# Kernel tuning notes

Hardware: AMD Instinct MI355X
Metric: run time of the kernel (lower is better)

Reference implementation:

```python
import jax, jax.numpy as jnp
import numpy as np

N = 100000   # nodes
E = 1600000  # edges
G = 64       # graphs in batch
D = 128      # node_dim
H = 128      # hid_dim
OUT = 10     # out_dim (classes)
L = 3        # max_layer GIN layers per branch
BN_EPS = 1e-5


def setup_inputs() -> dict:
    key = jax.random.key(0)
    ks = jax.random.split(key, 24)
    p = lambda k, shape: (jax.random.normal(k, shape, jnp.float32) * 0.05)
    inp = {
        "x": jax.random.normal(ks[0], (N, D), jnp.float32),
        "edge_index": jax.random.randint(ks[1], (2, E), 0, N, jnp.int32),
        "batch": jnp.sort(jax.random.randint(ks[2], (N,), 0, G, jnp.int32)),
        # branch A: conv1 + convs  (stacked per-layer params; node_dim == hid_dim)
        "W1a": p(ks[3], (L, D, H)), "b1a": p(ks[4], (L, H)),
        "W2a": p(ks[5], (L, H, H)), "b2a": p(ks[6], (L, H)),
        "ga": jnp.ones((L, H), jnp.float32), "bta": jnp.zeros((L, H), jnp.float32),
        # branch B: conv2 + convs2
        "W1b": p(ks[7], (L, D, H)), "b1b": p(ks[8], (L, H)),
        "W2b": p(ks[9], (L, H, H)), "b2b": p(ks[10], (L, H)),
        "gb": jnp.ones((L, H), jnp.float32), "btb": jnp.zeros((L, H), jnp.float32),
        # heads
        "lin1_w": p(ks[11], (2 * H, H)), "lin1_b": p(ks[12], (H,)),
        "lin2_w": p(ks[13], (H, OUT)), "lin2_b": p(ks[14], (OUT,)),
        # bilinear discriminator (nn.Bilinear(H, H, 1))
        "disc_w": p(ks[15], (H, H)), "disc_b": jnp.zeros((), jnp.float32),
    }
    return inp


def _gin(h, src, dst, W1, b1, W2, b2, g, bt):
    # GINConv (eps=0): MLP(x + sum_{j->i} x_j); MLP = Lin-ReLU-Lin-ReLU-BN
    agg = jax.ops.segment_sum(h[src], dst, num_segments=N)  # scatter-add over edges
    h = h + agg
    h = jax.nn.relu(h @ W1 + b1)
    h = jax.nn.relu(h @ W2 + b2)
    mu = h.mean(0)
    var = jnp.mean((h - mu) ** 2, axis=0)
    return (h - mu) * jax.lax.rsqrt(var + BN_EPS) * g + bt


def reference(x, edge_index, batch, W1a, b1a, W2a, b2a, ga, bta,
              W1b, b1b, W2b, b2b, gb, btb, lin1_w, lin1_b, lin2_w, lin2_b,
              disc_w, disc_b):
    src, dst = edge_index[0], edge_index[1]
    counts = jnp.clip(jax.ops.segment_sum(jnp.ones((N,), x.dtype), batch, num_segments=G), 1.0)

    # branch A: conv1 + convs -> per-graph mean pool
    h = x
    for i in range(L):
        h = _gin(h, src, dst, W1a[i], b1a[i], W2a[i], b2a[i], ga[i], bta[i])
    mean_a = jax.ops.segment_sum(h, batch, num_segments=G) / counts[:, None]  # [G,H]

    # branch B (subgraph branch, run on the same graph): conv2 + convs2 -> pool
    hb = x
    for i in range(L):
        hb = _gin(hb, src, dst, W1b[i], b1b[i], W2b[i], b2b[i], gb[i], btb[i])
    pool_x = jax.ops.segment_sum(hb, batch, num_segments=G) / counts[:, None]  # [G,H]

    # MI discriminator: shuffle index as in Net.MI
    idx = jnp.arange(G - 1, -1, -1)
    idx = idx.at[G // 2].set(idx[G // 2 + 1])
    shuffled = pool_x[idx]
    bil = lambda a, c: jnp.einsum('gd,de,ge->g', a, disc_w, c) + disc_b
    logits = jnp.concatenate([bil(pool_x, pool_x), bil(pool_x, shuffled)])  # [2G]

    # classification head: cat(mean_pool, pool_x) -> lin1 -> relu -> lin2 -> log_softmax
    z = jnp.concatenate([mean_a, pool_x], axis=-1)
    z = jax.nn.relu(z @ lin1_w + lin1_b)
    z = z @ lin2_w + lin2_b
    predicts = jax.nn.log_softmax(z, axis=-1)  # [G,OUT]

    return jnp.concatenate([predicts.ravel(), logits.ravel()])  # [G*OUT + 2G]
```

## Files before the change

### kernel.cpp

```cpp
#include <hip/hip_runtime.h>
#include <hip/hip_bf16.h>

#define NN 100000
#define EE 1600000
#define GG 64
#define HH 128
#define LL 3
#define BN_EPS 1e-5f
#define NBUCK 196
#define BCAP 12288
#define PART_CHUNK 8192

typedef __attribute__((ext_vector_type(8))) short bf16x8;
typedef __attribute__((ext_vector_type(4))) float f32x4;
typedef unsigned int uint32;

__device__ __forceinline__ float bflo(uint32 u) { return __uint_as_float(u << 16); }
__device__ __forceinline__ float bfhi(uint32 u) { return __uint_as_float(u & 0xffff0000u); }
__device__ __forceinline__ unsigned short f2bf(float f) {
    uint32 x = __float_as_uint(f);
    uint32 r = (x + 0x7fffu + ((x >> 16) & 1u)) >> 16;
    return (unsigned short)r;
}
__device__ __forceinline__ float bf2f(unsigned short u) { return __uint_as_float(((uint32)u) << 16); }
__device__ __forceinline__ void acc2(float2& a, uint32 u) { a.x += bflo(u); a.y += bfhi(u); }
__device__ __forceinline__ void accq(float4& a, uint32 u, float sc) {
    a.x += sc * (float)(u & 0xffu);
    a.y += sc * (float)((u >> 8) & 0xffu);
    a.z += sc * (float)((u >> 16) & 0xffu);
    a.w += sc * (float)(u >> 24);
}

__global__ __launch_bounds__(256) void partition_kernel(
    const int* __restrict__ src, const int* __restrict__ dst,
    int* __restrict__ bcnt, uint32* __restrict__ part) {
    __shared__ int cnt[NBUCK];
    __shared__ int loff[NBUCK + 1];
    __shared__ int gpos[NBUCK];
    __shared__ int lcur[NBUCK];
    __shared__ uint32 buf[PART_CHUNK];
    int tid = threadIdx.x;
    int base = blockIdx.x * PART_CHUNK;
    int n = min(PART_CHUNK, EE - base);
    for (int i = tid; i < NBUCK; i += 256) { cnt[i] = 0; lcur[i] = 0; }
    __syncthreads();
    for (int i = tid; i < n; i += 256) atomicAdd(&cnt[dst[base + i] >> 9], 1);
    __syncthreads();
    if (tid == 0) {
        int acc = 0;
        for (int b = 0; b < NBUCK; ++b) { loff[b] = acc; acc += cnt[b]; }
        loff[NBUCK] = acc;
    }
    __syncthreads();
    if (tid < NBUCK && cnt[tid] > 0) gpos[tid] = atomicAdd(&bcnt[tid], cnt[tid]);
    __syncthreads();
    for (int i = tid; i < n; i += 256) {
        int d = dst[base + i];
        int s = src[base + i];
        int b = d >> 9;
        int slot = atomicAdd(&lcur[b], 1);
        buf[loff[b] + slot] = (uint32)s | ((uint32)(d & 511) << 17);
    }
    __syncthreads();
    for (int i = tid; i < n; i += 256) {
        int lo = 0, hi = NBUCK;
        while (hi - lo > 1) { int mid = (lo + hi) >> 1; if (loff[mid] <= i) lo = mid; else hi = mid; }
        part[(size_t)lo * BCAP + gpos[lo] + (i - loff[lo])] = buf[i];
    }
}

__global__ __launch_bounds__(256) void build_col_kernel(
    const uint32* __restrict__ part, const int* __restrict__ bcnt,
    int* __restrict__ col, int2* __restrict__ rowpair) {
    __shared__ int ldeg[512];
    __shared__ int loffn[512];
    __shared__ int lcur[512];
    __shared__ int pscan[256];
    __shared__ int cl[BCAP];
    int b = blockIdx.x;
    int tid = threadIdx.x;
    int node0 = b << 9;
    int nn = min(node0 + 512, NN) - node0;
    int cnt = bcnt[b];
    int base = b * BCAP;
    const uint32* pp = part + (size_t)base;
    for (int i = tid; i < 512; i += 256) { ldeg[i] = 0; lcur[i] = 0; }
    __syncthreads();
    for (int i = tid; i < cnt; i += 256) atomicAdd(&ldeg[pp[i] >> 17], 1);
    __syncthreads();
    int t2 = tid * 2;
    int a0 = ldeg[t2], a1 = ldeg[t2 + 1];
    int ps = a0 + a1;
    pscan[tid] = ps;
    __syncthreads();
    for (int off = 1; off < 256; off <<= 1) {
        int v = (tid >= off) ? pscan[tid - off] : 0;
        __syncthreads();
        pscan[tid] += v;
        __syncthreads();
    }
    int eo = pscan[tid] - ps;
    loffn[t2] = eo;
    loffn[t2 + 1] = eo + a0;
    if (t2 < nn)     rowpair[node0 + t2]     = make_int2(base + eo, base + eo + a0);
    if (t2 + 1 < nn) rowpair[node0 + t2 + 1] = make_int2(base + eo + a0, base + eo + a0 + a1);
    __syncthreads();
    for (int i = tid; i < cnt; i += 256) {
        uint32 v = pp[i];
        int dl = (int)(v >> 17);
        int pos = atomicAdd(&lcur[dl], 1);
        cl[loffn[dl] + pos] = (int)(v & 0x1FFFFu);
    }
    __syncthreads();
    for (int i = tid; i < cnt; i += 256) col[base + i] = cl[i];
}

__global__ void counts_kernel(const int* __restrict__ batch, float* __restrict__ cnt, int n) {
    __shared__ int h[GG];
    int tid = threadIdx.x;
    if (tid < GG) h[tid] = 0;
    __syncthreads();
    int i = blockIdx.x * 256 + tid;
    if (i < n) atomicAdd(&h[batch[i]], 1);
    __syncthreads();
    if (tid < GG && h[tid]) atomicAdd(&cnt[tid], (float)h[tid]);
}

__global__ void x_to_bf16_kernel(const float* __restrict__ x, uint32* __restrict__ xb) {
    int i = blockIdx.x * 256 + threadIdx.x;
    if (i < NN * 32) {
        float4 v = ((const float4*)x)[i];
        uint2 o;
        o.x = (uint32)f2bf(v.x) | ((uint32)f2bf(v.y) << 16);
        o.y = (uint32)f2bf(v.z) | ((uint32)f2bf(v.w) << 16);
        ((uint2*)xb)[i] = o;
    }
}

#define MAT_STRIDE 16384

__global__ void convert_w_kernel(const float* __restrict__ W1a, const float* __restrict__ W2a,
                                 const float* __restrict__ W1b, const float* __restrict__ W2b,
                                 unsigned short* __restrict__ out) {
    int t = blockIdx.x * 256 + threadIdx.x;
    if (t >= 24576) return;
    int lane = t & 63;
    int r = t >> 6;
    int ks = r & 3; r >>= 2;
    int nt = r & 7; r >>= 3;
    int mat = r & 1; r >>= 1;
    int l = r % 3, br = r / 3;
    const float* W = br ? (mat ? W2b : W1b) : (mat ? W2a : W1a);
    const float* Wl = W + (size_t)l * 128 * 128;
    int n0 = nt * 16 + (lane & 15);
    int k0 = ks * 32 + (lane >> 4) * 8;
    unsigned short tmp[8];
#pragma unroll
    for (int j = 0; j < 8; ++j) tmp[j] = f2bf(Wl[(size_t)(k0 + j) * 128 + n0]);
    size_t seq = (size_t)(br * 3 + l) * 2 + mat;
    size_t off = (((seq * 8 + nt) * 4 + ks) * 64 + (size_t)lane) * 8;
    *(uint4*)(out + off) = *(const uint4*)tmp;
}

__global__ void gather0_kernel(const uint4* __restrict__ h4, const int2* __restrict__ rowpair,
                               const int* __restrict__ col, uint4* __restrict__ out) {
    int gw = (blockIdx.x * blockDim.x + threadIdx.x) >> 6;
    int lane = threadIdx.x & 63;
    if (gw >= NN) return;
    int slot = lane >> 4;
    int c8 = lane & 15;
    float2 acc[4] = {{0.f,0.f},{0.f,0.f},{0.f,0.f},{0.f,0.f}};
    if (slot == 0) {
        uint4 s = h4[(size_t)gw * 16 + c8];
        acc2(acc[0], s.x); acc2(acc[1], s.y); acc2(acc[2], s.z); acc2(acc[3], s.w);
    }
    int2 be = rowpair[gw];
    int beg = be.x, end = be.y;
    int e = beg;
    for (; e + 8 <= end; e += 8) {
        int j0 = col[e + slot], j1 = col[e + 4 + slot];
        uint4 u0 = h4[(size_t)j0 * 16 + c8];
        uint4 u1 = h4[(size_t)j1 * 16 + c8];
        acc2(acc[0], u0.x); acc2(acc[1], u0.y); acc2(acc[2], u0.z); acc2(acc[3], u0.w);
        acc2(acc[0], u1.x); acc2(acc[1], u1.y); acc2(acc[2], u1.z); acc2(acc[3], u1.w);
    }
    for (; e + 4 <= end; e += 4) {
        int j = col[e + slot];
        uint4 u = h4[(size_t)j * 16 + c8];
        acc2(acc[0], u.x); acc2(acc[1], u.y); acc2(acc[2], u.z); acc2(acc[3], u.w);
    }
    int rem = end - e;
    if (slot < rem) {
        int j = col[e + slot];
        uint4 u = h4[(size_t)j * 16 + c8];
        acc2(acc[0], u.x); acc2(acc[1], u.y); acc2(acc[2], u.z); acc2(acc[3], u.w);
    }
#pragma unroll
    for (int k = 0; k < 4; ++k) {
        acc[k].x += __shfl_xor(acc[k].x, 16); acc[k].y += __shfl_xor(acc[k].y, 16);
        acc[k].x += __shfl_xor(acc[k].x, 32); acc[k].y += __shfl_xor(acc[k].y, 32);
    }
    if (slot == 0) {
        uint4 r;
        r.x = (uint32)f2bf(acc[0].x) | ((uint32)f2bf(acc[0].y) << 16);
        r.y = (uint32)f2bf(acc[1].x) | ((uint32)f2bf(acc[1].y) << 16);
        r.z = (uint32)f2bf(acc[2].x) | ((uint32)f2bf(acc[2].y) << 16);
        r.w = (uint32)f2bf(acc[3].x) | ((uint32)f2bf(acc[3].y) << 16);
        out[(size_t)gw * 16 + c8] = r;
    }
}

__global__ void gather_dual_kernel(const uint32* __restrict__ y8, const float* __restrict__ scales,
                                   const int2* __restrict__ rowpair, const int* __restrict__ col,
                                   const float* __restrict__ stats,
                                   const float* __restrict__ ga, const float* __restrict__ bta,
                                   const float* __restrict__ gb, const float* __restrict__ btb,
                                   int lprev, uint2* __restrict__ out) {
    int gw = (blockIdx.x * blockDim.x + threadIdx.x) >> 6;
    int lane = threadIdx.x & 63;
    if (gw >= NN) return;
    int br = lane >> 5;
    const float* st = stats + (size_t)(lprev * 2 + br) * 256;
    const float* gmp = (br ? gb : ga) + lprev * 128;
    const float* btp = (br ? btb : bta) + lprev * 128;
    int cc0 = (lane * 4) & 127;
    float A[4], B[4];
#pragma unroll
    for (int j = 0; j < 4; ++j) {
        float s = st[cc0 + j], sq = st[128 + cc0 + j];
        float mu = s * (1.f / NN);
        float var = sq * (1.f / NN) - mu * mu;
        float a = gmp[cc0 + j] * rsqrtf(var + BN_EPS);
        A[j] = a;
        B[j] = btp[cc0 + j] - mu * a;
    }
    float4 accA = {0.f, 0.f, 0.f, 0.f};
    float4 accB = {0.f, 0.f, 0.f, 0.f};
    {
        uint32 us = y8[(size_t)gw * 64 + lane];
        float ss = scales[gw * 2 + br];
        accq(accA, us, ss);
    }
    int2 be = rowpair[gw];
    int beg = be.x, end = be.y;
    float degp1 = (float)(end - beg + 1);
    int e = beg;
    for (; e + 4 <= end; e += 4) {
        int j0 = col[e], j1 = col[e + 1], j2 = col[e + 2], j3 = col[e + 3];
        uint32 u0 = y8[(size_t)j0 * 64 + lane]; float s0 = scales[j0 * 2 + br];
        uint32 u1 = y8[(size_t)j1 * 64 + lane]; float s1 = scales[j1 * 2 + br];
        uint32 u2 = y8[(size_t)j2 * 64 + lane]; float s2 = scales[j2 * 2 + br];
        uint32 u3 = y8[(size_t)j3 * 64 + lane]; float s3 = scales[j3 * 2 + br];
        accq(accA, u0, s0);
        accq(accB, u1, s1);
        accq(accA, u2, s2);
        accq(accB, u3, s3);
    }
    for (; e < end; ++e) {
        int j = col[e];
        uint32 u = y8[(size_t)j * 64 + lane];
        float s = scales[j * 2 + br];
        accq(accA, u, s);
    }
    float o0 = A[0] * (accA.x + accB.x) + B[0] * degp1;
    float o1 = A[1] * (accA.y + accB.y) + B[1] * degp1;
    float o2 = A[2] * (accA.z + accB.z) + B[2] * degp1;
    float o3 = A[3] * (accA.w + accB.w) + B[3] * degp1;
    uint2 o;
    o.x = (uint32)f2bf(o0) | ((uint32)f2bf(o1) << 16);
    o.y = (uint32)f2bf(o2) | ((uint32)f2bf(o3) << 16);
    out[(size_t)gw * 64 + lane] = o;
}

__global__ __launch_bounds__(256, 2) void mlp_dual_kernel(
    const unsigned short* __restrict__ X, int in_stride, int in_off_mul,
    const unsigned short* __restrict__ wf_all,
    const float* __restrict__ b1a, const float* __restrict__ b1b,
    const float* __restrict__ b2a, const float* __restrict__ b2b,
    int l, int quant,
    unsigned short* __restrict__ Y, unsigned char* __restrict__ Y8,
    float* __restrict__ scales, float* __restrict__ stats, int n) {
    __shared__ unsigned short w1s[MAT_STRIDE];
    __shared__ unsigned short hs[4][16][136];
    __shared__ float ssum[128], ssq[128];

    int br = blockIdx.y;
    const unsigned short* Wf = wf_all + (size_t)(br * 3 + l) * 2 * MAT_STRIDE;
    const float* b1 = (br ? b1b : b1a) + l * 128;
    const float* b2 = (br ? b2b : b2a) + l * 128;
    float* statsp = stats + (size_t)(l * 2 + br) * 256;
    int in_off = in_off_mul * br;

    int tid = threadIdx.x;
    int wv = tid >> 6, lane = tid & 63;
    int quad = lane >> 4, l16 = lane & 15;

    {
        const uint4* srcp = (const uint4*)Wf;
        uint4* dstp = (uint4*)w1s;
        for (int i = tid; i < 2048; i += 256) dstp[i] = srcp[i];
    }
    if (tid < 128) { ssum[tid] = 0.f; ssq[tid] = 0.f; }
    __syncthreads();

    const bf16x8* w2g = (const bf16x8*)(Wf + MAT_STRIDE);
    unsigned char* hs8 = (unsigned char*)&hs[wv][0][0];

#pragma unroll
    for (int t = 0; t < 2; ++t) {
        int rowT = blockIdx.x * 128 + t * 64 + wv * 16;

        bf16x8 aF[4];
        {
            int r = rowT + l16;
            if (r >= n) r = n - 1;
            const unsigned short* xrow = X + (size_t)r * in_stride + in_off;
#pragma unroll
            for (int ks = 0; ks < 4; ++ks) aF[ks] = *(const bf16x8*)(xrow + ks * 32 + quad * 8);
        }

        f32x4 acc1[8];
#pragma unroll
        for (int nt = 0; nt < 8; ++nt) {
            f32x4 c = {0.f, 0.f, 0.f, 0.f};
#pragma unroll
            for (int ks = 0; ks < 4; ++ks) {
                bf16x8 bfrag = *(const bf16x8*)(&w1s[((nt * 4 + ks) * 64 + lane) * 8]);
                c = __builtin_amdgcn_mfma_f32_16x16x32_bf16(aF[ks], bfrag, c, 0, 0, 0);
            }
            acc1[nt] = c;
        }

#pragma unroll
        for (int nt = 0; nt < 8; ++nt) {
            int c0 = nt * 16 + l16;
            float bb = b1[c0];
#pragma unroll
            for (int r = 0; r < 4; ++r) {
                float v = fmaxf(acc1[nt][r] + bb, 0.f);
                hs[wv][quad * 4 + r][c0] = f2bf(v);
            }
        }

        bf16x8 aH[4];
#pragma unroll
        for (int ks = 0; ks < 4; ++ks)
            aH[ks] = *(const bf16x8*)(&hs[wv][l16][ks * 32 + quad * 8]);

        f32x4 acc2_[8];
#pragma unroll
        for (int nt = 0; nt < 8; ++nt) {
            bf16x8 bf0 = w2g[(nt * 4 + 0) * 64 + lane];
            bf16x8 bf1 = w2g[(nt * 4 + 1) * 64 + lane];
            bf16x8 bf2 = w2g[(nt * 4 + 2) * 64 + lane];
            bf16x8 bf3 = w2g[(nt * 4 + 3) * 64 + lane];
            f32x4 c = {0.f, 0.f, 0.f, 0.f};
            c = __builtin_amdgcn_mfma_f32_16x16x32_bf16(aH[0], bf0, c, 0, 0, 0);
            c = __builtin_amdgcn_mfma_f32_16x16x32_bf16(aH[1], bf1, c, 0, 0, 0);
            c = __builtin_amdgcn_mfma_f32_16x16x32_bf16(aH[2], bf2, c, 0, 0, 0);
            c = __builtin_amdgcn_mfma_f32_16x16x32_bf16(aH[3], bf3, c, 0, 0, 0);
            acc2_[nt] = c;
        }

#pragma unroll
        for (int nt = 0; nt < 8; ++nt) {
            int c0 = nt * 16 + l16;
            float bb = b2[c0];
            float s = 0.f, sq = 0.f;
#pragma unroll
            for (int r = 0; r < 4; ++r) {
                float v = fmaxf(acc2_[nt][r] + bb, 0.f);
                if (rowT + quad * 4 + r >= n) v = 0.f;
                acc2_[nt][r] = v;
                s += v; sq += v * v;
            }
            s += __shfl_xor(s, 16); s += __shfl_xor(s, 32);
            sq += __shfl_xor(sq, 16); sq += __shfl_xor(sq, 32);
            if (quad == 0) { atomicAdd(&ssum[c0], s); atomicAdd(&ssq[c0], sq); }
        }

        if (!quant) {
#pragma unroll
            for (int nt = 0; nt < 8; ++nt) {
                int c0 = nt * 16 + l16;
#pragma unroll
                for (int r = 0; r < 4; ++r) hs[wv][quad * 4 + r][c0] = f2bf(acc2_[nt][r]);
            }
            int grow = rowT + l16;
            if (grow < n) {
#pragma unroll
                for (int j = 0; j < 4; ++j) {
                    uint4 v = *(const uint4*)(&hs[wv][l16][quad * 32 + j * 8]);
                    *(uint4*)(Y + (size_t)grow * 256 + br * 128 + quad * 32 + j * 8) = v;
                }
            }
        } else {
#pragma unroll
            for (int r = 0; r < 4; ++r) {
                float m = acc2_[0][r];
#pragma unroll
                for (int nt = 1; nt < 8; ++nt) m = fmaxf(m, acc2_[nt][r]);
                m = fmaxf(m, __shfl_xor(m, 1));
                m = fmaxf(m, __shfl_xor(m, 2));
                m = fmaxf(m, __shfl_xor(m, 4));
                m = fmaxf(m, __shfl_xor(m, 8));
                float sc = m * (1.f / 255.f);
                float inv = (m > 0.f) ? 255.f / m : 0.f;
                int grow = rowT + quad * 4 + r;
                if (l16 == r && grow < n) scales[grow * 2 + br] = sc;
#pragma unroll
                for (int nt = 0; nt < 8; ++nt) {
                    uint32 u = (uint32)__float2int_rn(acc2_[nt][r] * inv);
                    hs8[(quad * 4 + r) * 144 + nt * 16 + l16] = (unsigned char)u;
                }
            }
            int grow = rowT + l16;
            if (grow < n) {
                *(uint4*)(Y8 + (size_t)grow * 256 + br * 128 + quad * 32) =
                    *(const uint4*)(hs8 + l16 * 144 + quad * 32);
                *(uint4*)(Y8 + (size_t)grow * 256 + br * 128 + quad * 32 + 16) =
                    *(const uint4*)(hs8 + l16 * 144 + quad * 32 + 16);
            }
        }
    }
    __syncthreads();
    if (tid < 128) {
        atomicAdd(&statsp[tid], ssum[tid]);
        atomicAdd(&statsp[128 + tid], ssq[tid]);
    }
}

#define POOL_CHUNK 128
__global__ void pool_dual_kernel(const unsigned short* __restrict__ h,
                                 const float* __restrict__ stats,
                                 const float* __restrict__ ga, const float* __restrict__ bta,
                                 const float* __restrict__ gb, const float* __restrict__ btb,
                                 const int* __restrict__ batch,
                                 float* __restrict__ poolA, float* __restrict__ poolB, int n) {
    int t = threadIdx.x;
    int br = t >> 7, cc = t & 127;
    const float* st = stats + (size_t)(2 * 2 + br) * 256;
    float s = st[cc], sq = st[128 + cc];
    float mu = s * (1.f / NN);
    float var = sq * (1.f / NN) - mu * mu;
    float gm = (br ? gb : ga)[2 * 128 + cc];
    float a = gm * rsqrtf(var + BN_EPS);
    float b = (br ? btb : bta)[2 * 128 + cc] - mu * a;
    float* pool = br ? poolB : poolA;

    int i0 = blockIdx.x * POOL_CHUNK;
    if (i0 >= n) return;
    int i1 = min(i0 + POOL_CHUNK, n);
    float acc = 0.f;
    int cur = batch[i0];
    for (int i = i0; i < i1; ++i) {
        int g = batch[i];
        if (g != cur) {
            atomicAdd(&pool[cur * 128 + cc], acc);
            acc = 0.f;
            cur = g;
        }
        acc += a * bf2f(h[(size_t)i * 256 + t]) + b;
    }
    atomicAdd(&pool[cur * 128 + cc], acc);
}

__global__ void disc_kernel(const float* __restrict__ poolB, const float* __restrict__ cnt,
                            const float* __restrict__ W, const float* __restrict__ db,
                            float* __restrict__ out) {
    int g = blockIdx.x, e = threadIdx.x;
    __shared__ float rs[128], rh[128];
    float invc = 1.f / fmaxf(cnt[g], 1.f);
    int gs = (g == 32) ? 30 : (63 - g);
    float invcs = 1.f / fmaxf(cnt[gs], 1.f);
    const float* a = poolB + g * 128;
    float t = 0.f;
    for (int d = 0; d < 128; ++d) t += a[d] * W[d * 128 + e];
    t *= invc;
    rs[e] = t * poolB[g * 128 + e] * invc;
    rh[e] = t * poolB[gs * 128 + e] * invcs;
    __syncthreads();
    for (int s = 64; s > 0; s >>= 1) {
        if (e < s) { rs[e] += rs[e + s]; rh[e] += rh[e + s]; }
        __syncthreads();
    }
    if (e == 0) {
        out[GG * 10 + g] = rs[0] + db[0];
        out[GG * 10 + GG + g] = rh[0] + db[0];
    }
}

__global__ void head_kernel(const float* __restrict__ poolA, const float* __restrict__ poolB,
                            const float* __restrict__ cnt,
                            const float* __restrict__ w1, const float* __restrict__ b1,
                            const float* __restrict__ w2, const float* __restrict__ b2,
                            float* __restrict__ out) {
    int g = blockIdx.x, j = threadIdx.x;
    __shared__ float s1[128];
    __shared__ float s2[10];
    __shared__ float lse;
    float invc = 1.f / fmaxf(cnt[g], 1.f);
    const float* ma = poolA + g * 128;
    const float* px = poolB + g * 128;
    float acc = b1[j];
    for (int k = 0; k < 128; ++k) acc += ma[k] * invc * w1[k * 128 + j];
    for (int k = 0; k < 128; ++k) acc += px[k] * invc * w1[(128 + k) * 128 + j];
    s1[j] = fmaxf(acc, 0.f);
    __syncthreads();
    if (j < 10) {
        float a = b2[j];
        for (int k = 0; k < 128; ++k) a += s1[k] * w2[k * 10 + j];
        s2[j] = a;
    }
    __syncthreads();
    if (j == 0) {
        float m = s2[0];
        for (int o = 1; o < 10; ++o) m = fmaxf(m, s2[o]);
        float se = 0.f;
        for (int o = 0; o < 10; ++o) se += expf(s2[o] - m);
        lse = m + logf(se);
    }
    __syncthreads();
    if (j < 10) out[g * 10 + j] = s2[j] - lse;
}

extern "C" void kernel_launch(void* const* d_in, const int* in_sizes, int n_in,
                              void* d_out, int out_size, void* d_ws, size_t ws_size,
                              hipStream_t stream) {
    const float* x     = (const float*)d_in[0];
    const int*   ei    = (const int*)d_in[1];
    const int*   batch = (const int*)d_in[2];
    const float* W1a = (const float*)d_in[3];
    const float* b1a = (const float*)d_in[4];
    const float* W2a = (const float*)d_in[5];
    const float* b2a = (const float*)d_in[6];
    const float* ga  = (const float*)d_in[7];
    const float* bta = (const float*)d_in[8];
    const float* W1b = (const float*)d_in[9];
    const float* b1b = (const float*)d_in[10];
    const float* W2b = (const float*)d_in[11];
    const float* b2b = (const float*)d_in[12];
    const float* gb  = (const float*)d_in[13];
    const float* btb = (const float*)d_in[14];
    const float* lin1_w = (const float*)d_in[15];
    const float* lin1_b = (const float*)d_in[16];
    const float* lin2_w = (const float*)d_in[17];
    const float* lin2_b = (const float*)d_in[18];
    const float* disc_w = (const float*)d_in[19];
    const float* disc_b = (const float*)d_in[20];
    float* out = (float*)d_out;

    const int* src = ei;
    const int* dst = ei + EE;

    size_t o = 0;
    auto take = [&](size_t b) { size_t p = o; o = (o + b + 255) & ~(size_t)255; return p; };
    uint8_t* w = (uint8_t*)d_ws;
    size_t o_xb   = take((size_t)NN * 128 * 2);
    size_t o_g0   = take((size_t)NN * 128 * 2);
    size_t o_bufP = take((size_t)NN * 256 * 2);
    size_t o_gbuf = take((size_t)NN * 256 * 2);
    size_t o_y8   = take((size_t)NN * 256);
    size_t o_scal = take((size_t)NN * 2 * 4);
    size_t o_wf   = take((size_t)12 * MAT_STRIDE * 2);
    size_t o_col  = take((size_t)NBUCK * BCAP * 4);
    size_t o_part = take((size_t)NBUCK * BCAP * 4);
    size_t o_rowpair = take((size_t)NN * 8);
    size_t zero_begin = o;
    size_t o_bcnt   = take((size_t)NBUCK * 4);
    size_t o_stats  = take((size_t)6 * 256 * 4);
    size_t o_cnt    = take(GG * 4);
    size_t o_poolA  = take((size_t)GG * 128 * 4);
    size_t o_poolB  = take((size_t)GG * 128 * 4);
    size_t zero_end = o;

    uint32* xb = (uint32*)(w + o_xb);
    uint32* g0 = (uint32*)(w + o_g0);
    unsigned short* bufP = (unsigned short*)(w + o_bufP);
    unsigned short* gbuf = (unsigned short*)(w + o_gbuf);
    unsigned char* y8 = (unsigned char*)(w + o_y8);
    float* scales = (float*)(w + o_scal);
    unsigned short* wf = (unsigned short*)(w + o_wf);
    int* col = (int*)(w + o_col);
    uint32* part = (uint32*)(w + o_part);
    int2* rowpair = (int2*)(w + o_rowpair);
    int* bcnt = (int*)(w + o_bcnt);
    float* stats = (float*)(w + o_stats);
    float* cnt = (float*)(w + o_cnt);
    float* poolA = (float*)(w + o_poolA);
    float* poolB = (float*)(w + o_poolB);

    hipMemsetAsync(w + zero_begin, 0, zero_end - zero_begin, stream);

    x_to_bf16_kernel<<<(NN * 32 + 255) / 256, 256, 0, stream>>>(x, xb);
    convert_w_kernel<<<(24576 + 255) / 256, 256, 0, stream>>>(W1a, W2a, W1b, W2b, wf);

    partition_kernel<<<(EE + PART_CHUNK - 1) / PART_CHUNK, 256, 0, stream>>>(src, dst, bcnt, part);
    build_col_kernel<<<NBUCK, 256, 0, stream>>>(part, bcnt, col, rowpair);
    counts_kernel<<<(NN + 255) / 256, 256, 0, stream>>>(batch, cnt, NN);

    int gatherBlocks = (NN + 3) / 4;
    dim3 mlpGrid((NN + 127) / 128, 2);

    gather0_kernel<<<gatherBlocks, 256, 0, stream>>>((const uint4*)xb, rowpair, col, (uint4*)g0);

    mlp_dual_kernel<<<mlpGrid, 256, 0, stream>>>(
        (const unsigned short*)g0, 128, 0, wf, b1a, b1b, b2a, b2b, 0, 1,
        nullptr, y8, scales, stats, NN);
    gather_dual_kernel<<<gatherBlocks, 256, 0, stream>>>(
        (const uint32*)y8, scales, rowpair, col, stats, ga, bta, gb, btb, 0, (uint2*)gbuf);
    mlp_dual_kernel<<<mlpGrid, 256, 0, stream>>>(
        gbuf, 256, 128, wf, b1a, b1b, b2a, b2b, 1, 1,
        nullptr, y8, scales, stats, NN);
    gather_dual_kernel<<<gatherBlocks, 256, 0, stream>>>(
        (const uint32*)y8, scales, rowpair, col, stats, ga, bta, gb, btb, 1, (uint2*)gbuf);
    mlp_dual_kernel<<<mlpGrid, 256, 0, stream>>>(
        gbuf, 256, 128, wf, b1a, b1b, b2a, b2b, 2, 0,
        bufP, nullptr, nullptr, stats, NN);

    pool_dual_kernel<<<(NN + POOL_CHUNK - 1) / POOL_CHUNK, 256, 0, stream>>>(
        bufP, stats, ga, bta, gb, btb, batch, poolA, poolB, NN);
    disc_kernel<<<GG, 128, 0, stream>>>(poolB, cnt, disc_w, disc_b, out);
    head_kernel<<<GG, 128, 0, stream>>>(poolA, poolB, cnt, lin1_w, lin1_b, lin2_w, lin2_b, out);
}
```

Measured before the change: 758.5 us.

## Quantize input features to int8 for first gather; restructure MLP kernel tiling

The input features are now converted to per-row symmetric int8 with a float scale instead of bf16, which halves the bytes fetched per neighbor in the first aggregation gather. That gather is rewritten to use two edge slots of 32 lanes with signed dequantization. Separately, the MLP kernel stops staging W1 in shared memory, reads both weight matrices directly from global memory, and processes 64 rows per block instead of 128. It also raises the occupancy hint to 4 blocks per SM. This adds quantization error on the raw input features and shifts weight reads onto cache.

```diff
diff --git a/kernel.cpp b/kernel.cpp
--- a/kernel.cpp
+++ b/kernel.cpp
@@ -29,6 +29,12 @@
     a.y += sc * (float)((u >> 8) & 0xffu);
     a.z += sc * (float)((u >> 16) & 0xffu);
     a.w += sc * (float)(u >> 24);
+}
+__device__ __forceinline__ void accqs(float4& a, uint32 u, float sc) {
+    a.x += sc * (float)((int)(u << 24) >> 24);
+    a.y += sc * (float)((int)(u << 16) >> 24);
+    a.z += sc * (float)((int)(u << 8) >> 24);
+    a.w += sc * (float)((int)u >> 24);
 }
 
 __global__ __launch_bounds__(256) void partition_kernel(
@@ -126,15 +132,22 @@
     if (tid < GG && h[tid]) atomicAdd(&cnt[tid], (float)h[tid]);
 }
 
-__global__ void x_to_bf16_kernel(const float* __restrict__ x, uint32* __restrict__ xb) {
-    int i = blockIdx.x * 256 + threadIdx.x;
-    if (i < NN * 32) {
-        float4 v = ((const float4*)x)[i];
-        uint2 o;
-        o.x = (uint32)f2bf(v.x) | ((uint32)f2bf(v.y) << 16);
-        o.y = (uint32)f2bf(v.z) | ((uint32)f2bf(v.w) << 16);
-        ((uint2*)xb)[i] = o;
-    }
+__global__ void x_to_i8_kernel(const float* __restrict__ x, unsigned short* __restrict__ x8,
+                               float* __restrict__ sc0) {
+    int row = (blockIdx.x * 256 + threadIdx.x) >> 6;
+    int lane = threadIdx.x & 63;
+    if (row >= NN) return;
+    float2 v = ((const float2*)x)[(size_t)row * 64 + lane];
+    float m = fmaxf(fabsf(v.x), fabsf(v.y));
+#pragma unroll
+    for (int off = 1; off < 64; off <<= 1) m = fmaxf(m, __shfl_xor(m, off));
+    float scale = m * (1.f / 127.f);
+    float inv = (m > 0.f) ? 127.f / m : 0.f;
+    int b0 = __float2int_rn(v.x * inv);
+    int b1 = __float2int_rn(v.y * inv);
+    unsigned short pk = (unsigned short)((b0 & 0xff) | ((b1 & 0xff) << 8));
+    x8[(size_t)row * 64 + lane] = pk;
+    if (lane == 0) sc0[row] = scale;
 }
 
 #define MAT_STRIDE 16384
@@ -162,51 +175,43 @@
     *(uint4*)(out + off) = *(const uint4*)tmp;
 }
 
-__global__ void gather0_kernel(const uint4* __restrict__ h4, const int2* __restrict__ rowpair,
-                               const int* __restrict__ col, uint4* __restrict__ out) {
+__global__ void gather0_kernel(const uint32* __restrict__ x8, const float* __restrict__ sc0,
+                               const int2* __restrict__ rowpair, const int* __restrict__ col,
+                               uint2* __restrict__ out) {
     int gw = (blockIdx.x * blockDim.x + threadIdx.x) >> 6;
     int lane = threadIdx.x & 63;
     if (gw >= NN) return;
-    int slot = lane >> 4;
-    int c8 = lane & 15;
-    float2 acc[4] = {{0.f,0.f},{0.f,0.f},{0.f,0.f},{0.f,0.f}};
-    if (slot == 0) {
-        uint4 s = h4[(size_t)gw * 16 + c8];
-        acc2(acc[0], s.x); acc2(acc[1], s.y); acc2(acc[2], s.z); acc2(acc[3], s.w);
-    }
+    int slot = lane >> 5;
+    int c = lane & 31;
+    float4 acc = {0.f, 0.f, 0.f, 0.f};
+    if (slot == 0) accqs(acc, x8[(size_t)gw * 32 + c], sc0[gw]);
     int2 be = rowpair[gw];
     int beg = be.x, end = be.y;
     int e = beg;
-    for (; e + 8 <= end; e += 8) {
-        int j0 = col[e + slot], j1 = col[e + 4 + slot];
-        uint4 u0 = h4[(size_t)j0 * 16 + c8];
-        uint4 u1 = h4[(size_t)j1 * 16 + c8];
-        acc2(acc[0], u0.x); acc2(acc[1], u0.y); acc2(acc[2], u0.z); acc2(acc[3], u0.w);
-        acc2(acc[0], u1.x); acc2(acc[1], u1.y); acc2(acc[2], u1.z); acc2(acc[3], u1.w);
-    }
     for (; e + 4 <= end; e += 4) {
+        int j0 = col[e + slot], j1 = col[e + 2 + slot];
+        uint32 u0 = x8[(size_t)j0 * 32 + c]; float s0 = sc0[j0];
+        uint32 u1 = x8[(size_t)j1 * 32 + c]; float s1 = sc0[j1];
+        accqs(acc, u0, s0);
+        accqs(acc, u1, s1);
+    }
+    for (; e + 2 <= end; e += 2) {
         int j = col[e + slot];
-        uint4 u = h4[(size_t)j * 16 + c8];
-        acc2(acc[0], u.x); acc2(acc[1], u.y); acc2(acc[2], u.z); acc2(acc[3], u.w);
-    }
-    int rem = end - e;
-    if (slot < rem) {
-        int j = col[e + slot];
-        uint4 u = h4[(size_t)j * 16 + c8];
-        acc2(acc[0], u.x); acc2(acc[1], u.y); acc2(acc[2], u.z); acc2(acc[3], u.w);
-    }
-#pragma unroll
-    for (int k = 0; k < 4; ++k) {
-        acc[k].x += __shfl_xor(acc[k].x, 16); acc[k].y += __shfl_xor(acc[k].y, 16);
-        acc[k].x += __shfl_xor(acc[k].x, 32); acc[k].y += __shfl_xor(acc[k].y, 32);
-    }
+        accqs(acc, x8[(size_t)j * 32 + c], sc0[j]);
+    }
+    if (e < end && slot == 0) {
+        int j = col[e];
+        accqs(acc, x8[(size_t)j * 32 + c], sc0[j]);
+    }
+    acc.x += __shfl_xor(acc.x, 32);
+    acc.y += __shfl_xor(acc.y, 32);
+    acc.z += __shfl_xor(acc.z, 32);
+    acc.w += __shfl_xor(acc.w, 32);
     if (slot == 0) {
-        uint4 r;
-        r.x = (uint32)f2bf(acc[0].x) | ((uint32)f2bf(acc[0].y) << 16);
-        r.y = (uint32)f2bf(acc[1].x) | ((uint32)f2bf(acc[1].y) << 16);
-        r.z = (uint32)f2bf(acc[2].x) | ((uint32)f2bf(acc[2].y) << 16);
-        r.w = (uint32)f2bf(acc[3].x) | ((uint32)f2bf(acc[3].y) << 16);
-        out[(size_t)gw * 16 + c8] = r;
+        uint2 o;
+        o.x = (uint32)f2bf(acc.x) | ((uint32)f2bf(acc.y) << 16);
+        o.y = (uint32)f2bf(acc.z) | ((uint32)f2bf(acc.w) << 16);
+        out[(size_t)gw * 32 + c] = o;
     }
 }
 
@@ -272,7 +277,7 @@
     out[(size_t)gw * 64 + lane] = o;
 }
 
-__global__ __launch_bounds__(256, 2) void mlp_dual_kernel(
+__global__ __launch_bounds__(256, 4) void mlp_dual_kernel(
     const unsigned short* __restrict__ X, int in_stride, int in_off_mul,
     const unsigned short* __restrict__ wf_all,
     const float* __restrict__ b1a, const float* __restrict__ b1b,
@@ -280,7 +285,6 @@
     int l, int quant,
     unsigned short* __restrict__ Y, unsigned char* __restrict__ Y8,
     float* __restrict__ scales, float* __restrict__ stats, int n) {
-    __shared__ unsigned short w1s[MAT_STRIDE];
     __shared__ unsigned short hs[4][16][136];
     __shared__ float ssum[128], ssq[128];
 
@@ -295,132 +299,128 @@
     int wv = tid >> 6, lane = tid & 63;
     int quad = lane >> 4, l16 = lane & 15;
 
-    {
-        const uint4* srcp = (const uint4*)Wf;
-        uint4* dstp = (uint4*)w1s;
-        for (int i = tid; i < 2048; i += 256) dstp[i] = srcp[i];
-    }
     if (tid < 128) { ssum[tid] = 0.f; ssq[tid] = 0.f; }
     __syncthreads();
 
+    const bf16x8* w1g = (const bf16x8*)Wf;
     const bf16x8* w2g = (const bf16x8*)(Wf + MAT_STRIDE);
     unsigned char* hs8 = (unsigned char*)&hs[wv][0][0];
 
-#pragma unroll
-    for (int t = 0; t < 2; ++t) {
-        int rowT = blockIdx.x * 128 + t * 64 + wv * 16;
-
-        bf16x8 aF[4];
-        {
-            int r = rowT + l16;
-            if (r >= n) r = n - 1;
-            const unsigned short* xrow = X + (size_t)r * in_stride + in_off;
-#pragma unroll
-            for (int ks = 0; ks < 4; ++ks) aF[ks] = *(const bf16x8*)(xrow + ks * 32 + quad * 8);
+    int row0 = blockIdx.x * 64 + wv * 16;
+
+    bf16x8 aF[4];
+    {
+        int r = row0 + l16;
+        if (r >= n) r = n - 1;
+        const unsigned short* xrow = X + (size_t)r * in_stride + in_off;
+#pragma unroll
+        for (int ks = 0; ks < 4; ++ks) aF[ks] = *(const bf16x8*)(xrow + ks * 32 + quad * 8);
+    }
+
+    f32x4 acc1[8];
+#pragma unroll
+    for (int nt = 0; nt < 8; ++nt) {
+        bf16x8 bf0 = w1g[(nt * 4 + 0) * 64 + lane];
+        bf16x8 bf1 = w1g[(nt * 4 + 1) * 64 + lane];
+        bf16x8 bf2 = w1g[(nt * 4 + 2) * 64 + lane];
+        bf16x8 bf3 = w1g[(nt * 4 + 3) * 64 + lane];
+        f32x4 c = {0.f, 0.f, 0.f, 0.f};
+        c = __builtin_amdgcn_mfma_f32_16x16x32_bf16(aF[0], bf0, c, 0, 0, 0);
+        c = __builtin_amdgcn_mfma_f32_16x16x32_bf16(aF[1], bf1, c, 0, 0, 0);
+        c = __builtin_amdgcn_mfma_f32_16x16x32_bf16(aF[2], bf2, c, 0, 0, 0);
+        c = __builtin_amdgcn_mfma_f32_16x16x32_bf16(aF[3], bf3, c, 0, 0, 0);
+        acc1[nt] = c;
+    }
+
+#pragma unroll
+    for (int nt = 0; nt < 8; ++nt) {
+        int c0 = nt * 16 + l16;
+        float bb = b1[c0];
+#pragma unroll
+        for (int r = 0; r < 4; ++r) {
+            float v = fmaxf(acc1[nt][r] + bb, 0.f);
+            hs[wv][quad * 4 + r][c0] = f2bf(v);
         }
-
-        f32x4 acc1[8];
-#pragma unroll
-        for (int nt = 0; nt < 8; ++nt) {
-            f32x4 c = {0.f, 0.f, 0.f, 0.f};
-#pragma unroll
-            for (int ks = 0; ks < 4; ++ks) {
-                bf16x8 bfrag = *(const bf16x8*)(&w1s[((nt * 4 + ks) * 64 + lane) * 8]);
-                c = __builtin_amdgcn_mfma_f32_16x16x32_bf16(aF[ks], bfrag, c, 0, 0, 0);
-            }
-            acc1[nt] = c;
+    }
+
+    bf16x8 aH[4];
+#pragma unroll
+    for (int ks = 0; ks < 4; ++ks)
+        aH[ks] = *(const bf16x8*)(&hs[wv][l16][ks * 32 + quad * 8]);
+
+    f32x4 acc2_[8];
+#pragma unroll
+    for (int nt = 0; nt < 8; ++nt) {
+        bf16x8 bf0 = w2g[(nt * 4 + 0) * 64 + lane];
+        bf16x8 bf1 = w2g[(nt * 4 + 1) * 64 + lane];
+        bf16x8 bf2 = w2g[(nt * 4 + 2) * 64 + lane];
+        bf16x8 bf3 = w2g[(nt * 4 + 3) * 64 + lane];
+        f32x4 c = {0.f, 0.f, 0.f, 0.f};
+        c = __builtin_amdgcn_mfma_f32_16x16x32_bf16(aH[0], bf0, c, 0, 0, 0);
+        c = __builtin_amdgcn_mfma_f32_16x16x32_bf16(aH[1], bf1, c, 0, 0, 0);
+        c = __builtin_amdgcn_mfma_f32_16x16x32_bf16(aH[2], bf2, c, 0, 0, 0);
+        c = __builtin_amdgcn_mfma_f32_16x16x32_bf16(aH[3], bf3, c, 0, 0, 0);
+        acc2_[nt] = c;
+    }
+
+#pragma unroll
+    for (int nt = 0; nt < 8; ++nt) {
+        int c0 = nt * 16 + l16;
+        float bb = b2[c0];
+        float s = 0.f, sq = 0.f;
+#pragma unroll
+        for (int r = 0; r < 4; ++r) {
+            float v = fmaxf(acc2_[nt][r] + bb, 0.f);
+            if (row0 + quad * 4 + r >= n) v = 0.f;
+            acc2_[nt][r] = v;
+            s += v; sq += v * v;
         }
-
+        s += __shfl_xor(s, 16); s += __shfl_xor(s, 32);
+        sq += __shfl_xor(sq, 16); sq += __shfl_xor(sq, 32);
+        if (quad == 0) { atomicAdd(&ssum[c0], s); atomicAdd(&ssq[c0], sq); }
+    }
+
+    if (!quant) {
 #pragma unroll
         for (int nt = 0; nt < 8; ++nt) {
             int c0 = nt * 16 + l16;
-            float bb = b1[c0];
-#pragma unroll
-            for (int r = 0; r < 4; ++r) {
-                float v = fmaxf(acc1[nt][r] + bb, 0.f);
-                hs[wv][quad * 4 + r][c0] = f2bf(v);
+#pragma unroll
+            for (int r = 0; r < 4; ++r) hs[wv][quad * 4 + r][c0] = f2bf(acc2_[nt][r]);
+        }
+        int grow = row0 + l16;
+        if (grow < n) {
+#pragma unroll
+            for (int j = 0; j < 4; ++j) {
+                uint4 v = *(const uint4*)(&hs[wv][l16][quad * 32 + j * 8]);
+                *(uint4*)(Y + (size_t)grow * 256 + br * 128 + quad * 32 + j * 8) = v;
             }
         }
-
-        bf16x8 aH[4];
-#pragma unroll
-        for (int ks = 0; ks < 4; ++ks)
-            aH[ks] = *(const bf16x8*)(&hs[wv][l16][ks * 32 + quad * 8]);
-
-        f32x4 acc2_[8];
-#pragma unroll
-        for (int nt = 0; nt < 8; ++nt) {
-            bf16x8 bf0 = w2g[(nt * 4 + 0) * 64 + lane];
-            bf16x8 bf1 = w2g[(nt * 4 + 1) * 64 + lane];
-            bf16x8 bf2 = w2g[(nt * 4 + 2) * 64 + lane];
-            bf16x8 bf3 = w2g[(nt * 4 + 3) * 64 + lane];
-            f32x4 c = {0.f, 0.f, 0.f, 0.f};
-            c = __builtin_amdgcn_mfma_f32_16x16x32_bf16(aH[0], bf0, c, 0, 0, 0);
-            c = __builtin_amdgcn_mfma_f32_16x16x32_bf16(aH[1], bf1, c, 0, 0, 0);
-            c = __builtin_amdgcn_mfma_f32_16x16x32_bf16(aH[2], bf2, c, 0, 0, 0);
-            c = __builtin_amdgcn_mfma_f32_16x16x32_bf16(aH[3], bf3, c, 0, 0, 0);
-            acc2_[nt] = c;
+    } else {
+#pragma unroll
+        for (int r = 0; r < 4; ++r) {
+            float m = acc2_[0][r];
+#pragma unroll
+            for (int nt = 1; nt < 8; ++nt) m = fmaxf(m, acc2_[nt][r]);
+            m = fmaxf(m, __shfl_xor(m, 1));
+            m = fmaxf(m, __shfl_xor(m, 2));
+            m = fmaxf(m, __shfl_xor(m, 4));
+            m = fmaxf(m, __shfl_xor(m, 8));
+            float sc = m * (1.f / 255.f);
+            float inv = (m > 0.f) ? 255.f / m : 0.f;
+            int grow = row0 + quad * 4 + r;
+            if (l16 == r && grow < n) scales[grow * 2 + br] = sc;
+#pragma unroll
+            for (int nt = 0; nt < 8; ++nt) {
+                uint32 u = (uint32)__float2int_rn(acc2_[nt][r] * inv);
+                hs8[(quad * 4 + r) * 144 + nt * 16 + l16] = (unsigned char)u;
+            }
         }
-
-#pragma unroll
-        for (int nt = 0; nt < 8; ++nt) {
-            int c0 = nt * 16 + l16;
-            float bb = b2[c0];
-            float s = 0.f, sq = 0.f;
-#pragma unroll
-            for (int r = 0; r < 4; ++r) {
-                float v = fmaxf(acc2_[nt][r] + bb, 0.f);
-                if (rowT + quad * 4 + r >= n) v = 0.f;
-                acc2_[nt][r] = v;
-                s += v; sq += v * v;
-            }
-            s += __shfl_xor(s, 16); s += __shfl_xor(s, 32);
-            sq += __shfl_xor(sq, 16); sq += __shfl_xor(sq, 32);
-            if (quad == 0) { atomicAdd(&ssum[c0], s); atomicAdd(&ssq[c0], sq); }
-        }
-
-        if (!quant) {
-#pragma unroll
-            for (int nt = 0; nt < 8; ++nt) {
-                int c0 = nt * 16 + l16;
-#pragma unroll
-                for (int r = 0; r < 4; ++r) hs[wv][quad * 4 + r][c0] = f2bf(acc2_[nt][r]);
-            }
-            int grow = rowT + l16;
-            if (grow < n) {
-#pragma unroll
-                for (int j = 0; j < 4; ++j) {
-                    uint4 v = *(const uint4*)(&hs[wv][l16][quad * 32 + j * 8]);
-                    *(uint4*)(Y + (size_t)grow * 256 + br * 128 + quad * 32 + j * 8) = v;
-                }
-            }
-        } else {
-#pragma unroll
-            for (int r = 0; r < 4; ++r) {
-                float m = acc2_[0][r];
-#pragma unroll
-                for (int nt = 1; nt < 8; ++nt) m = fmaxf(m, acc2_[nt][r]);
-                m = fmaxf(m, __shfl_xor(m, 1));
-                m = fmaxf(m, __shfl_xor(m, 2));
-                m = fmaxf(m, __shfl_xor(m, 4));
-                m = fmaxf(m, __shfl_xor(m, 8));
-                float sc = m * (1.f / 255.f);
-                float inv = (m > 0.f) ? 255.f / m : 0.f;
-                int grow = rowT + quad * 4 + r;
-                if (l16 == r && grow < n) scales[grow * 2 + br] = sc;
-#pragma unroll
-                for (int nt = 0; nt < 8; ++nt) {
-                    uint32 u = (uint32)__float2int_rn(acc2_[nt][r] * inv);
-                    hs8[(quad * 4 + r) * 144 + nt * 16 + l16] = (unsigned char)u;
-                }
-            }
-            int grow = rowT + l16;
-            if (grow < n) {
-                *(uint4*)(Y8 + (size_t)grow * 256 + br * 128 + quad * 32) =
-                    *(const uint4*)(hs8 + l16 * 144 + quad * 32);
-                *(uint4*)(Y8 + (size_t)grow * 256 + br * 128 + quad * 32 + 16) =
-                    *(const uint4*)(hs8 + l16 * 144 + quad * 32 + 16);
-            }
+        int grow = row0 + l16;
+        if (grow < n) {
+            *(uint4*)(Y8 + (size_t)grow * 256 + br * 128 + quad * 32) =
+                *(const uint4*)(hs8 + l16 * 144 + quad * 32);
+            *(uint4*)(Y8 + (size_t)grow * 256 + br * 128 + quad * 32 + 16) =
+                *(const uint4*)(hs8 + l16 * 144 + quad * 32 + 16);
         }
     }
     __syncthreads();
@@ -556,7 +556,8 @@
     size_t o = 0;
     auto take = [&](size_t b) { size_t p = o; o = (o + b + 255) & ~(size_t)255; return p; };
     uint8_t* w = (uint8_t*)d_ws;
-    size_t o_xb   = take((size_t)NN * 128 * 2);
+    size_t o_x8   = take((size_t)NN * 128);
+    size_t o_sc0  = take((size_t)NN * 4);
     size_t o_g0   = take((size_t)NN * 128 * 2);
     size_t o_bufP = take((size_t)NN * 256 * 2);
     size_t o_gbuf = take((size_t)NN * 256 * 2);
@@ -574,7 +575,8 @@
     size_t o_poolB  = take((size_t)GG * 128 * 4);
     size_t zero_end = o;
 
-    uint32* xb = (uint32*)(w + o_xb);
+    unsigned short* x8 = (unsigned short*)(w + o_x8);
+    float* sc0 = (float*)(w + o_sc0);
     uint32* g0 = (uint32*)(w + o_g0);
     unsigned short* bufP = (unsigned short*)(w + o_bufP);
     unsigned short* gbuf = (unsigned short*)(w + o_gbuf);
@@ -592,7 +594,7 @@
 
     hipMemsetAsync(w + zero_begin, 0, zero_end - zero_begin, stream);
 
-    x_to_bf16_kernel<<<(NN * 32 + 255) / 256, 256, 0, stream>>>(x, xb);
+    x_to_i8_kernel<<<(NN * 64 + 255) / 256, 256, 0, stream>>>(x, x8, sc0);
     convert_w_kernel<<<(24576 + 255) / 256, 256, 0, stream>>>(W1a, W2a, W1b, W2b, wf);
 
     partition_kernel<<<(EE + PART_CHUNK - 1) / PART_CHUNK, 256, 0, stream>>>(src, dst, bcnt, part);
@@ -600,9 +602,9 @@
     counts_kernel<<<(NN + 255) / 256, 256, 0, stream>>>(batch, cnt, NN);
 
     int gatherBlocks = (NN + 3) / 4;
-    dim3 mlpGrid((NN + 127) / 128, 2);
-
-    gather0_kernel<<<gatherBlocks, 256, 0, stream>>>((const uint4*)xb, rowpair, col, (uint4*)g0);
+    dim3 mlpGrid((NN + 63) / 64, 2);
+
+    gather0_kernel<<<gatherBlocks, 256, 0, stream>>>((const uint32*)x8, sc0, rowpair, col, (uint2*)g0);
 
     mlp_dual_kernel<<<mlpGrid, 256, 0, stream>>>(
         (const unsigned short*)g0, 128, 0, wf, b1a, b1b, b2a, b2b, 0, 1,
```

Result: slower. 795.7 us (+4.9%).
